# Performance work log

Hardware: AMD Instinct MI355X
Metric: run time of the kernel (lower is better)

## Reference

```python
import jax, jax.numpy as jnp
import numpy as np

N = 100000          # total nodes
G = 128             # number of graphs
D_IN, D_H, D_OUT = 512, 1024, 512
E = 1600000         # edges (unused by the math, matches forward signature)


def setup_inputs() -> dict:
    key = jax.random.key(0)
    ks = jax.random.split(key, 9)
    x = jax.random.normal(ks[0], (N, D_IN), dtype=jnp.float32)
    edge_index = jax.random.randint(ks[1], (2, E), 0, N, dtype=jnp.int64)
    # sorted batch ids; guarantee every graph id appears at least once
    batch = jnp.sort(jnp.concatenate([
        jnp.arange(G, dtype=jnp.int64),
        jax.random.randint(ks[2], (N - G,), 0, G, dtype=jnp.int64),
    ]))
    s = 0.02
    W0 = jax.random.normal(ks[3], (D_IN, D_H), dtype=jnp.float32) * s
    b0 = jnp.zeros((D_H,), dtype=jnp.float32)
    W1 = jax.random.normal(ks[4], (D_H, D_H), dtype=jnp.float32) * s
    b1 = jnp.zeros((D_H,), dtype=jnp.float32)
    W2 = jax.random.normal(ks[5], (D_H, D_OUT), dtype=jnp.float32) * s
    b2 = jnp.zeros((D_OUT,), dtype=jnp.float32)
    return {"x": x, "edge_index": edge_index, "batch": batch,
            "W0": W0, "b0": b0, "W1": W1, "b1": b1, "W2": W2, "b2": b2}


def reference(x, edge_index, batch, W0, b0, W1, b1, W2, b2):
    # Linear + ReLU stack (dropout p=0 -> identity in eval). edge_index is unused,
    # matching the original module (its 'GCN' layer is a plain nn.Linear).
    h = jax.nn.relu(x @ W0 + b0)
    h = jax.nn.relu(h @ W1 + b1)
    h = jax.nn.relu(h @ W2 + b2)        # [N, D_OUT]
    # global mean pool per graph: fused segment-sum replaces the per-graph mask loop
    sums = jax.ops.segment_sum(h, batch, num_segments=G)                 # [G, D_OUT]
    counts = jax.ops.segment_sum(jnp.ones((h.shape[0],), h.dtype), batch,
                                 num_segments=G)                          # [G]
    return sums / counts[:, None]
```

## Files before the change

### kernel.cpp

```cpp
#include <hip/hip_runtime.h>
#include <cstdint>
#include <cstddef>

typedef __bf16 bf16x8 __attribute__((ext_vector_type(8)));
typedef float f32x4 __attribute__((ext_vector_type(4)));

__device__ __forceinline__ unsigned short f2bf(float f) {
  unsigned u = __float_as_uint(f);
  u += 0x7fffu + ((u >> 16) & 1u);
  return (unsigned short)(u >> 16);
}
__device__ __forceinline__ float bf2f(unsigned short s) {
  return __uint_as_float(((unsigned)s) << 16);
}

__device__ __forceinline__ void gld_lds16(const void* g, void* l) {
  __builtin_amdgcn_global_load_lds(
      (const __attribute__((address_space(1))) void*)g,
      (__attribute__((address_space(3))) void*)l, 16, 0, 0);
}

#define BARM() do { __builtin_amdgcn_s_barrier(); asm volatile("" ::: "memory"); } while (0)
#define VMCNT(n) asm volatile("s_waitcnt vmcnt(" #n ")" ::: "memory")
#define LGKM0()  do { asm volatile("s_waitcnt lgkmcnt(0)" ::: "memory"); \
                      __builtin_amdgcn_sched_barrier(0); } while (0)

__global__ void transpose_w(const float* __restrict__ w, unsigned short* __restrict__ wt,
                            int K, int N) {
  __shared__ float tile[32][33];
  int nt = N >> 5;
  int bx = blockIdx.x % nt;
  int by = blockIdx.x / nt;
  int tx = threadIdx.x & 31, ty = threadIdx.x >> 5;
#pragma unroll
  for (int r = 0; r < 32; r += 8)
    tile[ty + r][tx] = w[(size_t)(by * 32 + ty + r) * N + bx * 32 + tx];
  __syncthreads();
#pragma unroll
  for (int r = 0; r < 32; r += 8)
    wt[(size_t)(bx * 32 + ty + r) * K + by * 32 + tx] = f2bf(tile[tx][ty + r]);
}

__global__ void cvt_x(const float* __restrict__ x, unsigned short* __restrict__ xb,
                      int rows, int nvalid, int D) {
  size_t total = (size_t)rows * D / 8;
  for (size_t i = (size_t)blockIdx.x * blockDim.x + threadIdx.x; i < total;
       i += (size_t)gridDim.x * blockDim.x) {
    size_t e = i * 8;
    int row = (int)(e / (size_t)D);
    uint4 ov;
    if (row < nvalid) {
      const float4* s = (const float4*)(x + e);
      float4 v0 = s[0], v1 = s[1];
      ov.x = (unsigned)f2bf(v0.x) | ((unsigned)f2bf(v0.y) << 16);
      ov.y = (unsigned)f2bf(v0.z) | ((unsigned)f2bf(v0.w) << 16);
      ov.z = (unsigned)f2bf(v1.x) | ((unsigned)f2bf(v1.y) << 16);
      ov.w = (unsigned)f2bf(v1.z) | ((unsigned)f2bf(v1.w) << 16);
    } else {
      ov.x = ov.y = ov.z = ov.w = 0u;
    }
    *(uint4*)(xb + e) = ov;
  }
}

__device__ __forceinline__ bf16x8 read_frag(const unsigned short* region, int row, int kel) {
  int ke = kel ^ (((row >> 1) & 3) << 3);
  return *(const bf16x8*)(region + row * 32 + ke);
}

__device__ __forceinline__ void stage_half(const unsigned short* gpanel, int K, int kofs,
                                           unsigned short* region, int tid) {
  int row = tid >> 2;
  int ke = ((tid & 3) * 8) ^ (((row >> 1) & 3) << 3);
  gld_lds16(gpanel + (size_t)row * K + kofs + ke, region + tid * 8);
}

#define MFMA8(MB, BV)                                                           \
  do {                                                                          \
    __builtin_amdgcn_s_setprio(1);                                              \
    _Pragma("unroll") for (int mm = 0; mm < 2; ++mm) {                          \
      _Pragma("unroll") for (int nn = 0; nn < 4; ++nn)                          \
        acc[(MB) + mm][nn] = __builtin_amdgcn_mfma_f32_16x16x32_bf16(           \
            av[mm], BV[nn], acc[(MB) + mm][nn], 0, 0, 0);                       \
    }                                                                           \
    __builtin_amdgcn_s_setprio(0);                                              \
  } while (0)

#define GEMM_PREAMBLE_AND_KLOOP()                                               \
  const int tid = threadIdx.x;                                                  \
  const int w = tid >> 6, l = tid & 63;                                         \
  const int wm = w >> 2, wn = w & 3;                                            \
  const int lc = l & 15, lk8 = (l >> 4) * 8;                                    \
  const int nbn = N >> 8;                                                       \
  const int nwg = gridDim.x;                                                    \
  const int q = nwg >> 3, rr = nwg & 7;                                         \
  const int xcd = blockIdx.x & 7, ib = blockIdx.x >> 3;                         \
  const int bswz = (xcd < rr ? xcd * (q + 1) : rr * (q + 1) + (xcd - rr) * q) + ib; \
  const int bm = bswz / nbn, bn = bswz - bm * nbn;                              \
  const unsigned short* Ap = A + (size_t)bm * 256 * K;                          \
  const unsigned short* Bp = Bt + (size_t)bn * 256 * K;                         \
  const int T = K >> 6;                                                         \
  f32x4 acc[4][4] = {};                                                         \
  stage_half(Ap, K, 0, &lds[0][0][0][0][0], tid);                               \
  stage_half(Bp, K, 0, &lds[0][1][0][0][0], tid);                               \
  stage_half(Ap, K, 32, &lds[0][0][1][0][0], tid);                              \
  stage_half(Bp, K, 32, &lds[0][1][1][0][0], tid);                              \
  stage_half(Ap, K, 64, &lds[1][0][0][0][0], tid);                              \
  stage_half(Bp, K, 64, &lds[1][1][0][0][0], tid);                              \
  VMCNT(2);                                                                     \
  BARM();                                                                       \
  for (int t = 0; t < T; ++t) {                                                 \
    const int s = t & 1;                                                        \
    const unsigned short* Ak0 = &lds[s][0][0][0][0];                            \
    const unsigned short* Ak1 = &lds[s][0][1][0][0];                            \
    const unsigned short* Bk0 = &lds[s][1][0][0][0];                            \
    const unsigned short* Bk1 = &lds[s][1][1][0][0];                            \
    unsigned short* nAk1 = &lds[s ^ 1][0][1][0][0];                             \
    unsigned short* nBk1 = &lds[s ^ 1][1][1][0][0];                             \
    unsigned short* cAk0 = &lds[s][0][0][0][0];                                 \
    unsigned short* cBk0 = &lds[s][1][0][0][0];                                 \
    bf16x8 av[2], b0[4], b1[4];                                                 \
                                    \
    _Pragma("unroll") for (int mm = 0; mm < 2; ++mm)                            \
        av[mm] = read_frag(Ak0, wm * 64 + mm * 16 + lc, lk8);                   \
    _Pragma("unroll") for (int nn = 0; nn < 4; ++nn)                            \
        b0[nn] = read_frag(Bk0, wn * 64 + nn * 16 + lc, lk8);                   \
    if (t + 1 < T) stage_half(Ap, K, (t + 1) * 64 + 32, nAk1, tid);             \
    BARM(); LGKM0(); MFMA8(0, b0); BARM();                                      \
                                           \
    _Pragma("unroll") for (int mm = 0; mm < 2; ++mm)                            \
        av[mm] = read_frag(Ak0, wm * 64 + (2 + mm) * 16 + lc, lk8);             \
    if (t + 1 < T) stage_half(Bp, K, (t + 1) * 64 + 32, nBk1, tid);             \
    BARM(); LGKM0(); MFMA8(2, b0); BARM();                                      \
                                    \
    _Pragma("unroll") for (int mm = 0; mm < 2; ++mm)                            \
        av[mm] = read_frag(Ak1, wm * 64 + mm * 16 + lc, lk8);                   \
    _Pragma("unroll") for (int nn = 0; nn < 4; ++nn)                            \
        b1[nn] = read_frag(Bk1, wn * 64 + nn * 16 + lc, lk8);                   \
    if (t + 2 < T) stage_half(Ap, K, (t + 2) * 64, cAk0, tid);                  \
    BARM(); LGKM0(); MFMA8(0, b1); BARM();                                      \
                          \
    _Pragma("unroll") for (int mm = 0; mm < 2; ++mm)                            \
        av[mm] = read_frag(Ak1, wm * 64 + (2 + mm) * 16 + lc, lk8);             \
    if (t + 2 < T) { stage_half(Bp, K, (t + 2) * 64, cBk0, tid); VMCNT(2); }    \
    else { VMCNT(0); }                                                          \
    BARM(); LGKM0(); MFMA8(2, b1); BARM();                                      \
  }

__global__ __launch_bounds__(1024, 1) void gemm256(
    const unsigned short* __restrict__ A,
    const unsigned short* __restrict__ Bt,
    const float* __restrict__ bias,
    unsigned short* __restrict__ C,
    int N, int K) {
  __shared__ alignas(16) unsigned short lds[2][2][2][256][32];
  GEMM_PREAMBLE_AND_KLOOP();

  unsigned short* eps = &lds[0][0][0][0][0];
  float bv[4];
#pragma unroll
  for (int nn = 0; nn < 4; ++nn) bv[nn] = bias[bn * 256 + wn * 64 + nn * 16 + lc];

#pragma unroll
  for (int r = 0; r < 2; ++r) {
    if ((wm >> 1) == r) {
#pragma unroll
      for (int mm = 0; mm < 4; ++mm) {
#pragma unroll
        for (int nn = 0; nn < 4; ++nn) {
          int lcol = wn * 64 + nn * 16 + lc;
#pragma unroll
          for (int j = 0; j < 4; ++j) {
            int lrow = (wm & 1) * 64 + mm * 16 + (l >> 4) * 4 + j;
            float v = fmaxf(acc[mm][nn][j] + bv[nn], 0.0f);
            eps[lrow * 256 + (lcol ^ (((lrow >> 2) & 3) << 4))] = f2bf(v);
          }
        }
      }
    }
    BARM();
#pragma unroll
    for (int it = 0; it < 4; ++it) {
      int flat = it * 1024 + tid;
      int lrow = flat >> 5, cb = flat & 31;
      int ce = (cb * 8) ^ (((lrow >> 2) & 3) << 4);
      uint4 v = *(const uint4*)&eps[lrow * 256 + ce];
      *(uint4*)&C[(size_t)(bm * 256 + r * 128 + lrow) * N + bn * 256 + cb * 8] = v;
    }
    BARM();
  }
}

__global__ __launch_bounds__(1024, 1) void gemm_pool(
    const unsigned short* __restrict__ A,
    const unsigned short* __restrict__ Bt,
    const float* __restrict__ bias,
    const int* __restrict__ batch,
    float* __restrict__ part,
    int N, int K, int row0, int Nn) {
  __shared__ alignas(16) unsigned short lds[2][2][2][256][32];
  GEMM_PREAMBLE_AND_KLOOP();

  unsigned short* eps = &lds[0][0][0][0][0];
  int* batchLS = (int*)&lds[1][0][0][0][0];
  if (tid < 256) {
    int grow = row0 + bm * 256 + tid;
    batchLS[tid] = (grow < Nn) ? batch[grow] : -1;
  }
  float bv[4];
#pragma unroll
  for (int nn = 0; nn < 4; ++nn) bv[nn] = bias[bn * 256 + wn * 64 + nn * 16 + lc];

#pragma unroll
  for (int r = 0; r < 2; ++r) {
    if ((wm >> 1) == r) {
#pragma unroll
      for (int mm = 0; mm < 4; ++mm) {
#pragma unroll
        for (int nn = 0; nn < 4; ++nn) {
          int lcol = wn * 64 + nn * 16 + lc;
#pragma unroll
          for (int j = 0; j < 4; ++j) {
            int lrow = (wm & 1) * 64 + mm * 16 + (l >> 4) * 4 + j;
            float v = fmaxf(acc[mm][nn][j] + bv[nn], 0.0f);
            eps[lrow * 256 + (lcol ^ (((lrow >> 2) & 3) << 4))] = f2bf(v);
          }
        }
      }
    }
    BARM();
    {
      int col = tid & 255;
      int qt = tid >> 8;
      int gcur = -2;
      float run = 0.f;
      int gcolbase = bn * 256 + col;
      for (int i = 0; i < 32; ++i) {
        int lr = qt * 32 + i;
        int g = batchLS[r * 128 + lr];
        if (g != gcur) {
          if (gcur >= 0) atomicAdd(&part[(size_t)gcur * N + gcolbase], run);
          gcur = g; run = 0.f;
        }
        run += bf2f(eps[lr * 256 + (col ^ (((lr >> 2) & 3) << 4))]);
      }
      if (gcur >= 0) atomicAdd(&part[(size_t)gcur * N + gcolbase], run);
    }
    BARM();
  }
}

__global__ void zero_part(float* __restrict__ part, int n) {
  int i = blockIdx.x * blockDim.x + threadIdx.x;
  if (i < n) part[i] = 0.f;
}

__global__ void pool_div(const float* __restrict__ part, const int* __restrict__ batch,
                         float* __restrict__ out, int n, int D, int G) {
  int idx = blockIdx.x * blockDim.x + threadIdx.x;
  if (idx >= G * D) return;
  int g = idx / D;
  int lo, hi;
  { int a = 0, b = n; while (a < b) { int m = (a + b) >> 1; if (batch[m] < g) a = m + 1; else b = m; } lo = a; }
  { int a = lo, b = n; while (a < b) { int m = (a + b) >> 1; if (batch[m] < g + 1) a = m + 1; else b = m; } hi = a; }
  out[idx] = part[idx] / (float)(hi - lo);
}

static inline size_t align256(size_t x) { return (x + 255) & ~(size_t)255; }

extern "C" void kernel_launch(void* const* d_in, const int* in_sizes, int n_in,
                              void* d_out, int out_size, void* d_ws, size_t ws_size,
                              hipStream_t stream) {
  const float* x = (const float*)d_in[0];
  const int* batch = (const int*)d_in[2];
  const float* W0 = (const float*)d_in[3];
  const float* b0 = (const float*)d_in[4];
  const float* W1 = (const float*)d_in[5];
  const float* b1 = (const float*)d_in[6];
  const float* W2 = (const float*)d_in[7];
  const float* b2 = (const float*)d_in[8];
  float* out = (float*)d_out;

  const int Nn = in_sizes[2];
  const int DIN = 512, DH = 1024, DOUT = 512;
  const int G = out_size / DOUT;
  const int Mpad = ((Nn + 255) / 256) * 256;

  uint8_t* p = (uint8_t*)d_ws;
  unsigned short* W0t = (unsigned short*)p; p += align256((size_t)DH * DIN * 2);
  unsigned short* W1t = (unsigned short*)p; p += align256((size_t)DH * DH * 2);
  unsigned short* W2t = (unsigned short*)p; p += align256((size_t)DOUT * DH * 2);
  float* part         = (float*)p;          p += align256((size_t)G * DOUT * 4);
  size_t used = (size_t)(p - (uint8_t*)d_ws);
  size_t avail = ws_size > used ? ws_size - used : 0;
  size_t per_row = (size_t)(DIN + DH + DH) * 2;
  long long chl = (long long)(avail / per_row);
  chl = (chl / 256) * 256;
  int CH = (int)(chl < 256 ? 256 : chl);
  if (CH > Mpad) CH = Mpad;
  unsigned short* xb = (unsigned short*)p; p += align256((size_t)CH * DIN * 2);
  unsigned short* h0 = (unsigned short*)p; p += align256((size_t)CH * DH * 2);
  unsigned short* h1 = (unsigned short*)p; p += align256((size_t)CH * DH * 2);

  zero_part<<<dim3((G * DOUT + 255) / 256), 256, 0, stream>>>(part, G * DOUT);

  transpose_w<<<dim3((DIN / 32) * (DH / 32)), 256, 0, stream>>>(W0, W0t, DIN, DH);
  transpose_w<<<dim3((DH / 32) * (DH / 32)), 256, 0, stream>>>(W1, W1t, DH, DH);
  transpose_w<<<dim3((DH / 32) * (DOUT / 32)), 256, 0, stream>>>(W2, W2t, DH, DOUT);

  for (int off = 0; off < Mpad; off += CH) {
    int rows = Mpad - off; if (rows > CH) rows = CH;
    int nvalid = Nn - off;
    size_t cvt_threads = (size_t)rows * DIN / 8;
    int cvt_blocks = (int)((cvt_threads + 255) / 256);
    if (cvt_blocks > 2048) cvt_blocks = 2048;
    cvt_x<<<dim3(cvt_blocks), 256, 0, stream>>>(x + (size_t)off * DIN, xb, rows, nvalid, DIN);

    gemm256<<<dim3((rows / 256) * (DH / 256)), 1024, 0, stream>>>(xb, W0t, b0, h0, DH, DIN);
    gemm256<<<dim3((rows / 256) * (DH / 256)), 1024, 0, stream>>>(h0, W1t, b1, h1, DH, DH);
    gemm_pool<<<dim3((rows / 256) * (DOUT / 256)), 1024, 0, stream>>>(
        h1, W2t, b2, batch, part, DOUT, DH, off, Nn);
  }

  pool_div<<<dim3((G * DOUT + 255) / 256), 256, 0, stream>>>(part, batch, out, Nn, DOUT, G);
}
```

Baseline: 659.3 us.

## Merge four k-loop phases into two with 16-MFMA blocks and fewer barriers

```diff
diff --git a/kernel.cpp b/kernel.cpp
--- a/kernel.cpp
+++ b/kernel.cpp
@@ -22,8 +22,7 @@
 
 #define BARM() do { __builtin_amdgcn_s_barrier(); asm volatile("" ::: "memory"); } while (0)
 #define VMCNT(n) asm volatile("s_waitcnt vmcnt(" #n ")" ::: "memory")
-#define LGKM0()  do { asm volatile("s_waitcnt lgkmcnt(0)" ::: "memory"); \
-                      __builtin_amdgcn_sched_barrier(0); } while (0)
+#define LGKMW() asm volatile("s_waitcnt lgkmcnt(0)" ::: "memory")
 
 __global__ void transpose_w(const float* __restrict__ w, unsigned short* __restrict__ wt,
                             int K, int N) {
@@ -75,16 +74,11 @@
   gld_lds16(gpanel + (size_t)row * K + kofs + ke, region + tid * 8);
 }
 
-#define MFMA8(MB, BV)                                                           \
-  do {                                                                          \
-    __builtin_amdgcn_s_setprio(1);                                              \
-    _Pragma("unroll") for (int mm = 0; mm < 2; ++mm) {                          \
+#define MFMA16X(BV)                                                             \
+  _Pragma("unroll") for (int mm = 0; mm < 4; ++mm)                              \
       _Pragma("unroll") for (int nn = 0; nn < 4; ++nn)                          \
-        acc[(MB) + mm][nn] = __builtin_amdgcn_mfma_f32_16x16x32_bf16(           \
-            av[mm], BV[nn], acc[(MB) + mm][nn], 0, 0, 0);                       \
-    }                                                                           \
-    __builtin_amdgcn_s_setprio(0);                                              \
-  } while (0)
+          acc[mm][nn] = __builtin_amdgcn_mfma_f32_16x16x32_bf16(                \
+              av[mm], BV[nn], acc[mm][nn], 0, 0, 0)
 
 #define GEMM_PREAMBLE_AND_KLOOP()                                               \
   const int tid = threadIdx.x;                                                  \
@@ -119,32 +113,32 @@
     unsigned short* nBk1 = &lds[s ^ 1][1][1][0][0];                             \
     unsigned short* cAk0 = &lds[s][0][0][0][0];                                 \
     unsigned short* cBk0 = &lds[s][1][0][0][0];                                 \
-    bf16x8 av[2], b0[4], b1[4];                                                 \
-                                    \
-    _Pragma("unroll") for (int mm = 0; mm < 2; ++mm)                            \
+    bf16x8 av[4], bq[4];                                                        \
+                                                     \
+    _Pragma("unroll") for (int mm = 0; mm < 4; ++mm)                            \
         av[mm] = read_frag(Ak0, wm * 64 + mm * 16 + lc, lk8);                   \
     _Pragma("unroll") for (int nn = 0; nn < 4; ++nn)                            \
-        b0[nn] = read_frag(Bk0, wn * 64 + nn * 16 + lc, lk8);                   \
-    if (t + 1 < T) stage_half(Ap, K, (t + 1) * 64 + 32, nAk1, tid);             \
-    BARM(); LGKM0(); MFMA8(0, b0); BARM();                                      \
-                                           \
-    _Pragma("unroll") for (int mm = 0; mm < 2; ++mm)                            \
-        av[mm] = read_frag(Ak0, wm * 64 + (2 + mm) * 16 + lc, lk8);             \
-    if (t + 1 < T) stage_half(Bp, K, (t + 1) * 64 + 32, nBk1, tid);             \
-    BARM(); LGKM0(); MFMA8(2, b0); BARM();                                      \
-                                    \
-    _Pragma("unroll") for (int mm = 0; mm < 2; ++mm)                            \
+        bq[nn] = read_frag(Bk0, wn * 64 + nn * 16 + lc, lk8);                   \
+    if (t + 1 < T) {                                                            \
+      stage_half(Ap, K, (t + 1) * 64 + 32, nAk1, tid);                          \
+      stage_half(Bp, K, (t + 1) * 64 + 32, nBk1, tid);                          \
+    }                                                                           \
+    MFMA16X(bq);                                                                \
+    LGKMW();                                                                    \
+    BARM();               \
+                                                     \
+    _Pragma("unroll") for (int mm = 0; mm < 4; ++mm)                            \
         av[mm] = read_frag(Ak1, wm * 64 + mm * 16 + lc, lk8);                   \
     _Pragma("unroll") for (int nn = 0; nn < 4; ++nn)                            \
-        b1[nn] = read_frag(Bk1, wn * 64 + nn * 16 + lc, lk8);                   \
-    if (t + 2 < T) stage_half(Ap, K, (t + 2) * 64, cAk0, tid);                  \
-    BARM(); LGKM0(); MFMA8(0, b1); BARM();                                      \
-                          \
-    _Pragma("unroll") for (int mm = 0; mm < 2; ++mm)                            \
-        av[mm] = read_frag(Ak1, wm * 64 + (2 + mm) * 16 + lc, lk8);             \
-    if (t + 2 < T) { stage_half(Bp, K, (t + 2) * 64, cBk0, tid); VMCNT(2); }    \
-    else { VMCNT(0); }                                                          \
-    BARM(); LGKM0(); MFMA8(2, b1); BARM();                                      \
+        bq[nn] = read_frag(Bk1, wn * 64 + nn * 16 + lc, lk8);                   \
+    if (t + 2 < T) {                                                            \
+      stage_half(Ap, K, (t + 2) * 64, cAk0, tid);                               \
+      stage_half(Bp, K, (t + 2) * 64, cBk0, tid);                               \
+    }                                                                           \
+    MFMA16X(bq);                                                                \
+    LGKMW();                                                                    \
+    if (t + 2 < T) { VMCNT(2); } else { VMCNT(0); }                             \
+    BARM();            \
   }
 
 __global__ __launch_bounds__(1024, 1) void gemm256(
```

Result: no change. 647.7 us, median of 2 (-1.8%).
